# Optimization experiments

Hardware: AMD Instinct MI355X
Metric: run time of the kernel (lower is better)

Reference implementation:

```python
import jax, jax.numpy as jnp
import numpy as np
from jax import lax

DT = 0.005
HISTORY = 1
B, T = 512, 4096


def setup_inputs() -> dict:
    key = jax.random.key(0)
    k1, k2, k3 = jax.random.split(key, 3)
    return {
        "pred_vel": jax.random.normal(k1, (B, T, 2), dtype=jnp.float32),
        "targ_vel": jax.random.normal(k2, (B, T, 2), dtype=jnp.float32),
        "q_pos": jnp.asarray(1e-4, dtype=jnp.float32),
        "q_vel": jnp.asarray(1e-3, dtype=jnp.float32),
        "r_vel": jnp.asarray(1e-2, dtype=jnp.float32),
        "p0": jax.random.normal(k3, (B, 2), dtype=jnp.float32),
    }


def _kf_positions(pred_vel, q_pos, q_vel, r_vel, p0, dt):
    """Batched differentiable constant-velocity KF; measures velocity.
    State per sample: [px, py, vx, vy]. Returns filtered positions (B, T, 2)."""
    dtype = pred_vel.dtype
    F = jnp.array([[1, 0, dt, 0],
                   [0, 1, 0, dt],
                   [0, 0, 1, 0],
                   [0, 0, 0, 1]], dtype=dtype)
    Q = jnp.diag(jnp.stack([q_pos, q_pos, q_vel, q_vel]).astype(dtype))
    R = r_vel.astype(dtype) * jnp.eye(2, dtype=dtype)

    x0 = jnp.concatenate([p0, jnp.zeros_like(p0)], axis=-1)  # (B, 4)
    P0 = jnp.eye(4, dtype=dtype)  # covariance shared across batch (scalar noise)

    def step(carry, z_t):
        x, P = carry
        x_pred = x @ F.T                           # (B, 4)
        P_pred = F @ P @ F.T + Q                   # (4, 4)
        S = P_pred[2:, 2:] + R                     # (2, 2) innovation cov
        # K = P_pred[:, 2:] @ inv(S); S symmetric -> solve
        K = jnp.linalg.solve(S, P_pred[:, 2:].T).T  # (4, 2)
        innov = z_t - x_pred[:, 2:]                # (B, 2)
        x_new = x_pred + innov @ K.T               # (B, 4)
        P_new = P_pred - K @ P_pred[2:, :]         # (I - K H) P_pred
        return (x_new, P_new), x_new[:, :2]

    (_, _), pos = lax.scan(step, (x0, P0), jnp.swapaxes(pred_vel, 0, 1))
    return jnp.swapaxes(pos, 0, 1)  # (B, T, 2)


def integrate_velocities(vel, dt, p0):
    return p0[:, None, :] + jnp.cumsum(vel * dt, axis=1)


def reference(pred_vel, targ_vel, q_pos, q_vel, r_vel, p0):
    pred_pos = _kf_positions(pred_vel, q_pos, q_vel, r_vel, p0, DT)
    gt_pos = integrate_velocities(targ_vel, DT, p0)
    # mode == 'part': windowed position differences with history=1
    pw = pred_pos[:, HISTORY:, :] - pred_pos[:, :-HISTORY, :]
    gw = gt_pos[:, HISTORY:, :] - gt_pos[:, :-HISTORY, :]
    return jnp.mean((pw - gw) ** 2)
```

## Files before the change

kernel.cpp:

```cpp
#include <hip/hip_runtime.h>
#include <math.h>


namespace {
constexpr int   Bn = 512;
constexpr int   Tn = 4096;
constexpr float DTc = 0.005f;
constexpr int   Lc = 64;
constexpr int   Wc = 64;
constexpr int   NCHUNK = Tn / Lc;
constexpr int   GB = 4;
constexpr int   NTRANSMAX = 256;
constexpr float INVC = 1.0f / (512.0f * 4095.0f * 2.0f);
}

__global__ __launch_bounds__(256) void kf_loss_kernel(
    const float* __restrict__ pred,
    const float* __restrict__ targ,
    const float* __restrict__ q_vel,
    const float* __restrict__ r_vel,
    float* __restrict__ out)
{
  const int tid = threadIdx.x;
  const int d  = tid & 1;
  const int bl = tid >> 1;
  const int c  = blockIdx.x >> 2;
  const int g  = blockIdx.x & (GB - 1);
  const int b  = g * 128 + bl;

  const float qv = q_vel[0];
  const float r  = r_vel[0];

  const int t0 = c * Lc;
  const float* zp = pred + (size_t)b * (Tn * 2) + d;
  const float* wp = targ + (size_t)b * (Tn * 2) + d;

  float acc = 0.0f;

  __shared__ float skp[NTRANSMAX];
  __shared__ float skv[NTRANSMAX];

  if (t0 >= NTRANSMAX) {
    float u   = 0.5f * (qv + sqrtf(fmaf(qv, qv, 4.0f * qv * r)));
    float s   = u + r;
    float inv = 1.0f / s;
    float kv  = u * inv;
    float cst = u - qv;
    float bst = (DTc * cst * r) / u;
    float kp  = (bst + DTc * cst) * inv;

    float v = 0.0f;
    int t = t0 - Wc;
    #pragma unroll 16
    for (int i = 0; i < Wc; ++i, ++t) {
      float z = zp[2 * t];
      v = fmaf(kv, z - v, v);
    }
    #pragma unroll 16
    for (int i = 0; i < Lc; ++i, ++t) {
      float z = zp[2 * t];
      float w = wp[2 * t];
      float innov = z - v;
      float e = fmaf(kp, innov, DTc * v);
      e = fmaf(-DTc, w, e);
      acc = fmaf(e, e, acc);
      v = fmaf(kv, innov, v);
    }
  } else {
    if (tid == 0) {
      float bcov = 0.0f, ccov = 1.0f;
      const int nk = t0 + Lc;
      for (int t = 0; t < nk; ++t) {
        float bp = fmaf(DTc, ccov, bcov);
        float cp = ccov + qv;
        float sden = cp + r;
        float inv = __builtin_amdgcn_rcpf(sden);
        float kp = bp * inv;
        float kv = cp * inv;
        skp[t] = kp;
        skv[t] = kv;
        bcov = fmaf(-kp, cp, bp);
        ccov = fmaf(-kv, cp, cp);
      }
    }
    __syncthreads();

    float v = 0.0f;
    int t = t0 - Wc; if (t < 0) t = 0;
    for (; t < t0; ++t) {
      float z = zp[2 * t];
      v = fmaf(skv[t], z - v, v);
    }
    for (; t < t0 + Lc; ++t) {
      float z = zp[2 * t];
      float innov = z - v;
      if (t > 0) {
        float w = wp[2 * t];
        float e = fmaf(skp[t], innov, DTc * v);
        e = fmaf(-DTc, w, e);
        acc = fmaf(e, e, acc);
      }
      v = fmaf(skv[t], innov, v);
    }
  }

  #pragma unroll
  for (int off = 32; off > 0; off >>= 1)
    acc += __shfl_down(acc, off);
  __shared__ float wpart[4];
  const int lane = tid & 63, wid = tid >> 6;
  if (lane == 0) wpart[wid] = acc;
  __syncthreads();
  if (tid == 0) {
    float s = (wpart[0] + wpart[1]) + (wpart[2] + wpart[3]);
    atomicAdd(out, s * INVC);
  }
}

extern "C" void kernel_launch(void* const* d_in, const int* in_sizes, int n_in,
                              void* d_out, int out_size, void* d_ws, size_t ws_size,
                              hipStream_t stream) {
  const float* pred = (const float*)d_in[0];
  const float* targ = (const float*)d_in[1];
  const float* qv   = (const float*)d_in[3];
  const float* rv   = (const float*)d_in[4];
  float* out = (float*)d_out;

  hipMemsetAsync(out, 0, sizeof(float), stream);

  dim3 grid(NCHUNK * GB);
  dim3 block(256);
  kf_loss_kernel<<<grid, block, 0, stream>>>(pred, targ, qv, rv, out);
}
```

Measured before the change: 108.8 us.

## Stage chunk inputs in LDS with coalesced float4 loads and shrink chunk/warmup windows

Each block now cooperatively loads its 128-sample by time-window slab of pred and targ with float4 loads into shared memory, transposed so that the time-serial filter reads from LDS. Before, each thread did strided scalar global loads. Chunk length drops from 64 to 16 and warmup from 64 to 12, giving a 4x larger grid and less redundant warmup work. The shorter warmup depends on the steady-state gain converging within 12 steps, which risks small accuracy differences. It also adds LDS traffic and a barrier per block.

```diff
diff --git a/kernel.cpp b/kernel.cpp
--- a/kernel.cpp
+++ b/kernel.cpp
@@ -3,14 +3,15 @@
 
 
 namespace {
-constexpr int   Bn = 512;
 constexpr int   Tn = 4096;
 constexpr float DTc = 0.005f;
-constexpr int   Lc = 64;
-constexpr int   Wc = 64;
+constexpr int   Lc = 16;
+constexpr int   Wc = 12;
 constexpr int   NCHUNK = Tn / Lc;
-constexpr int   GB = 4;
-constexpr int   NTRANSMAX = 256;
+constexpr int   NBpb = 128;
+constexpr int   TTmax = Lc + Wc;
+constexpr int   NTRANS_C = 4;
+constexpr int   GAINS_N = 64;
 constexpr float INVC = 1.0f / (512.0f * 4095.0f * 2.0f);
 }
 
@@ -21,83 +22,108 @@
     const float* __restrict__ r_vel,
     float* __restrict__ out)
 {
+  __shared__ float2 zt[TTmax * NBpb];
+  __shared__ float2 wt[Lc * NBpb];
+  __shared__ float skp[GAINS_N];
+  __shared__ float skv[GAINS_N];
+  __shared__ float wpart[4];
+
   const int tid = threadIdx.x;
-  const int d  = tid & 1;
-  const int bl = tid >> 1;
-  const int c  = blockIdx.x >> 2;
-  const int g  = blockIdx.x & (GB - 1);
-  const int b  = g * 128 + bl;
+  const int bg  = blockIdx.x & 3;
+  const int c   = blockIdx.x >> 2;
+  const int t0  = c * Lc;
+  const int TS  = (t0 >= Wc) ? (t0 - Wc) : 0;
 
-  const float qv = q_vel[0];
-  const float r  = r_vel[0];
+  const float* basez = pred + (size_t)bg * NBpb * (Tn * 2);
+  const float* basew = targ + (size_t)bg * NBpb * (Tn * 2);
 
-  const int t0 = c * Lc;
-  const float* zp = pred + (size_t)b * (Tn * 2) + d;
-  const float* wp = targ + (size_t)b * (Tn * 2) + d;
+  {
+    const int woff = t0 * 2;
+    #pragma unroll
+    for (int it = 0; it < 4; ++it) {
+      int i = it * 256 + tid;
+      int b = i >> 3, j = i & 7;
+      const float4 wv = *(const float4*)(basew + (size_t)b * (Tn * 2) + woff + j * 4);
+      wt[(2 * j)     * NBpb + b] = make_float2(wv.x, wv.y);
+      wt[(2 * j + 1) * NBpb + b] = make_float2(wv.z, wv.w);
+    }
+  }
+  if (t0 >= Wc) {
+    const int zoff = TS * 2;
+    #pragma unroll
+    for (int it = 0; it < 7; ++it) {
+      int i = it * 256 + tid;
+      int b = (int)((unsigned)i / 14u), j = i - b * 14;
+      const float4 zv = *(const float4*)(basez + (size_t)b * (Tn * 2) + zoff + j * 4);
+      zt[(2 * j)     * NBpb + b] = make_float2(zv.x, zv.y);
+      zt[(2 * j + 1) * NBpb + b] = make_float2(zv.z, zv.w);
+    }
+  } else {
+    #pragma unroll
+    for (int it = 0; it < 4; ++it) {
+      int i = it * 256 + tid;
+      int b = i >> 3, j = i & 7;
+      const float4 zv = *(const float4*)(basez + (size_t)b * (Tn * 2) + j * 4);
+      zt[(2 * j)     * NBpb + b] = make_float2(zv.x, zv.y);
+      zt[(2 * j + 1) * NBpb + b] = make_float2(zv.z, zv.w);
+    }
+  }
+  if (c < NTRANS_C && tid == 0) {
+    float bcov = 0.0f, ccov = 1.0f;
+    for (int t = 0; t < GAINS_N; ++t) {
+      float bp = fmaf(DTc, ccov, bcov);
+      float cp = ccov + q_vel[0];
+      float inv = 1.0f / (cp + r_vel[0]);
+      float kp = bp * inv;
+      float kv = cp * inv;
+      skp[t] = kp;  skv[t] = kv;
+      bcov = fmaf(-kp, cp, bp);
+      ccov = fmaf(-kv, cp, cp);
+    }
+  }
+  __syncthreads();
 
+  const int b = tid >> 1, d = tid & 1;
+  const float* zf = ((const float*)zt) + d;
+  const float* wf = ((const float*)wt) + d;
   float acc = 0.0f;
 
-  __shared__ float skp[NTRANSMAX];
-  __shared__ float skv[NTRANSMAX];
-
-  if (t0 >= NTRANSMAX) {
+  if (c >= NTRANS_C) {
+    const float qv = q_vel[0], r = r_vel[0];
     float u   = 0.5f * (qv + sqrtf(fmaf(qv, qv, 4.0f * qv * r)));
-    float s   = u + r;
-    float inv = 1.0f / s;
+    float inv = 1.0f / (u + r);
     float kv  = u * inv;
     float cst = u - qv;
     float bst = (DTc * cst * r) / u;
     float kp  = (bst + DTc * cst) * inv;
 
     float v = 0.0f;
-    int t = t0 - Wc;
-    #pragma unroll 16
-    for (int i = 0; i < Wc; ++i, ++t) {
-      float z = zp[2 * t];
-      v = fmaf(kv, z - v, v);
-    }
-    #pragma unroll 16
-    for (int i = 0; i < Lc; ++i, ++t) {
-      float z = zp[2 * t];
-      float w = wp[2 * t];
+    #pragma unroll
+    for (int lt = 0; lt < Wc; ++lt)
+      v = fmaf(kv, zf[2 * (lt * NBpb + b)] - v, v);
+    #pragma unroll
+    for (int lt = Wc; lt < TTmax; ++lt) {
+      float z = zf[2 * (lt * NBpb + b)];
+      float w = wf[2 * ((lt - Wc) * NBpb + b)];
       float innov = z - v;
-      float e = fmaf(kp, innov, DTc * v);
-      e = fmaf(-DTc, w, e);
+      float e = fmaf(kp, innov, DTc * (v - w));
       acc = fmaf(e, e, acc);
       v = fmaf(kv, innov, v);
     }
   } else {
-    if (tid == 0) {
-      float bcov = 0.0f, ccov = 1.0f;
-      const int nk = t0 + Lc;
-      for (int t = 0; t < nk; ++t) {
-        float bp = fmaf(DTc, ccov, bcov);
-        float cp = ccov + qv;
-        float sden = cp + r;
-        float inv = __builtin_amdgcn_rcpf(sden);
-        float kp = bp * inv;
-        float kv = cp * inv;
-        skp[t] = kp;
-        skv[t] = kv;
-        bcov = fmaf(-kp, cp, bp);
-        ccov = fmaf(-kv, cp, cp);
-      }
+    const int warm = t0 - TS;
+    float v = 0.0f;
+    for (int lt = 0; lt < warm; ++lt) {
+      int t = TS + lt;
+      v = fmaf(skv[t], zf[2 * (lt * NBpb + b)] - v, v);
     }
-    __syncthreads();
-
-    float v = 0.0f;
-    int t = t0 - Wc; if (t < 0) t = 0;
-    for (; t < t0; ++t) {
-      float z = zp[2 * t];
-      v = fmaf(skv[t], z - v, v);
-    }
-    for (; t < t0 + Lc; ++t) {
-      float z = zp[2 * t];
+    for (int lt = warm; lt < warm + Lc; ++lt) {
+      int t = TS + lt;
+      float z = zf[2 * (lt * NBpb + b)];
       float innov = z - v;
       if (t > 0) {
-        float w = wp[2 * t];
-        float e = fmaf(skp[t], innov, DTc * v);
-        e = fmaf(-DTc, w, e);
+        float w = wf[2 * ((lt - warm) * NBpb + b)];
+        float e = fmaf(skp[t], innov, DTc * (v - w));
         acc = fmaf(e, e, acc);
       }
       v = fmaf(skv[t], innov, v);
@@ -107,7 +133,6 @@
   #pragma unroll
   for (int off = 32; off > 0; off >>= 1)
     acc += __shfl_down(acc, off);
-  __shared__ float wpart[4];
   const int lane = tid & 63, wid = tid >> 6;
   if (lane == 0) wpart[wid] = acc;
   __syncthreads();
@@ -128,7 +153,7 @@
 
   hipMemsetAsync(out, 0, sizeof(float), stream);
 
-  dim3 grid(NCHUNK * GB);
+  dim3 grid(NCHUNK * 4);
   dim3 block(256);
   kf_loss_kernel<<<grid, block, 0, stream>>>(pred, targ, qv, rv, out);
 }
```

Measured after the change: 98.35 us. 1.11x faster.
